# Performance work log

Measured on AMD Instinct MI355X. Metric: run time of the kernel, lower is better.

The kernel has to match this reference:

```python
import jax, jax.numpy as jnp
import numpy as np

EPS = 1e-5

def _ln(x, g, b):
    mu = jnp.mean(x, axis=-1, keepdims=True)
    var = jnp.mean((x - mu) ** 2, axis=-1, keepdims=True)
    return (x - mu) * jax.lax.rsqrt(var + EPS) * g + b

B, SQ, SK, C, H = 4, 1024, 2048, 1024, 16
DH = C // H          # head_dim (latent_dim == in_dim)
L = C                # latent_dim

def setup_inputs() -> dict:
    key = jax.random.key(0)
    ks = list(jax.random.split(key, 16))
    s = 0.02
    d = {
        'queries': jax.random.normal(ks[0], (B, SQ, C), jnp.float32),
        'contexts': jax.random.normal(ks[1], (B, SK, C), jnp.float32),
        # SelfAttention params
        'sa_ln_g': jnp.ones((C,), jnp.float32),
        'sa_ln_b': jnp.zeros((C,), jnp.float32),
        'sa_qkv_w': jax.random.normal(ks[2], (2 * L + C, C), jnp.float32) * s,  # torch Linear weight (out,in)
        'sa_out_w': jax.random.normal(ks[3], (C, C), jnp.float32) * s,
        'sa_out_b': jnp.zeros((C,), jnp.float32),
        # Cross Attention params
        'ca_ln_g': jnp.ones((C,), jnp.float32),
        'ca_ln_b': jnp.zeros((C,), jnp.float32),
        'ca_q_w': jax.random.normal(ks[4], (L, C), jnp.float32) * s,
        'ca_k_w': jax.random.normal(ks[5], (L, C), jnp.float32) * s,
        'ca_v_w': jax.random.normal(ks[6], (C, C), jnp.float32) * s,
        'ca_out_w': jax.random.normal(ks[7], (C, C), jnp.float32) * s,
        'ca_out_b': jnp.zeros((C,), jnp.float32),
        # FFN (linear block) params
        'ff_ln1_g': jnp.ones((C,), jnp.float32),
        'ff_ln1_b': jnp.zeros((C,), jnp.float32),
        'ff_w1': jax.random.normal(ks[8], (2 * C, C), jnp.float32) * s,
        'ff_ln2_g': jnp.ones((2 * C,), jnp.float32),
        'ff_ln2_b': jnp.zeros((2 * C,), jnp.float32),
        'ff_w2': jax.random.normal(ks[9], (C, 2 * C), jnp.float32) * s,
    }
    return d

def _forward(queries, contexts, sa_ln_g, sa_ln_b, sa_qkv_w, sa_out_w, sa_out_b,
             ca_ln_g, ca_ln_b, ca_q_w, ca_k_w, ca_v_w, ca_out_w, ca_out_b,
             ff_ln1_g, ff_ln1_b, ff_w1, ff_ln2_g, ff_ln2_b, ff_w2):
    scale = 1.0 / jnp.sqrt(jnp.float32(C))  # note: module scales by sqrt(C), not sqrt(head_dim)
    # ---- SelfAttention ----
    x = queries
    h = _ln(x, sa_ln_g, sa_ln_b)
    qkv = (h @ sa_qkv_w.T).reshape(B, SQ, H, -1)  # (B,SQ,H, 2*DH + C//H)
    q, k, v = jnp.split(qkv, [DH, 2 * DH], axis=-1)
    e = jnp.einsum('nqhc,nkhc->nhqk', q, k)
    a = jax.nn.softmax(e * scale, axis=-1)
    o = jnp.einsum('nhql,nlhc->nqhc', a, v).reshape(B, SQ, C)
    x = o @ sa_out_w.T + sa_out_b + x
    # ---- Cross Attention ----
    qpre = x
    hq = _ln(x, ca_ln_g, ca_ln_b)
    q = (hq @ ca_q_w.T).reshape(B, SQ, H, DH)
    k = (contexts @ ca_k_w.T).reshape(B, SK, H, DH)
    v = (contexts @ ca_v_w.T).reshape(B, SK, H, C // H)
    energy = jnp.einsum('nqhc,nkhc->nhqk', q, k)  # (B,H,SQ,SK)
    a = jax.nn.softmax(energy * scale, axis=-1)
    o = jnp.einsum('nhql,nlhc->nqhc', a, v).reshape(B, SQ, C)
    x = o @ ca_out_w.T + ca_out_b + qpre
    # ---- FFN: LN -> SiLU -> Linear -> LN -> SiLU -> Linear, residual ----
    f = jax.nn.silu(_ln(x, ff_ln1_g, ff_ln1_b))
    f = f @ ff_w1.T
    f = jax.nn.silu(_ln(f, ff_ln2_g, ff_ln2_b))
    f = f @ ff_w2.T
    out = x + f  # dropout p=0 -> identity
    return out, energy

def reference(queries, contexts, sa_ln_g, sa_ln_b, sa_qkv_w, sa_out_w, sa_out_b,
              ca_ln_g, ca_ln_b, ca_q_w, ca_k_w, ca_v_w, ca_out_w, ca_out_b,
              ff_ln1_g, ff_ln1_b, ff_w1, ff_ln2_g, ff_ln2_b, ff_w2):
    return _forward(queries, contexts, sa_ln_g, sa_ln_b, sa_qkv_w, sa_out_w, sa_out_b,
                    ca_ln_g, ca_ln_b, ca_q_w, ca_k_w, ca_v_w, ca_out_w, ca_out_b,
                    ff_ln1_g, ff_ln1_b, ff_w1, ff_ln2_g, ff_ln2_b, ff_w2)
```

## Files before the change

### kernel.cpp

```cpp
#include <hip/hip_runtime.h>
#include <hip/hip_bf16.h>
#include <math.h>


namespace {
constexpr int BB  = 4;
constexpr int SQ_ = 1024;
constexpr int SK_ = 2048;
constexpr int CC  = 1024;
constexpr int HH  = 16;
constexpr float SCALE  = 0.03125f;
constexpr float LN_EPS = 1e-5f;
}

typedef __hip_bfloat16 bf16;
typedef __attribute__((ext_vector_type(8))) short short8;
typedef __attribute__((ext_vector_type(4))) float f32x4;

__device__ __forceinline__ void gload16(const void* g, void* l) {
    __builtin_amdgcn_global_load_lds((const __attribute__((address_space(1))) unsigned int*)g,
                                     (__attribute__((address_space(3))) unsigned int*)l,
                                     16, 0, 0);
}

#define MAXJOBS 10
struct CvtJobs {
    const float* src[MAXJOBS];
    bf16*        dst[MAXJOBS];
    int          end[MAXJOBS];
    int          njobs;
};

__global__ __launch_bounds__(256)
void cvt_all(CvtJobs J) {
    const int i = blockIdx.x * 256 + threadIdx.x;
    if (i >= J.end[J.njobs - 1]) return;
    int j = 0;
    while (i >= J.end[j]) ++j;
    const int base = j ? J.end[j - 1] : 0;
    const int k = i - base;
    const float4 a = ((const float4*)J.src[j])[2 * k];
    const float4 b = ((const float4*)J.src[j])[2 * k + 1];
    union { ushort4 v; bf16 h[4]; } lo, hi;
    lo.h[0] = __float2bfloat16(a.x); lo.h[1] = __float2bfloat16(a.y);
    lo.h[2] = __float2bfloat16(a.z); lo.h[3] = __float2bfloat16(a.w);
    hi.h[0] = __float2bfloat16(b.x); hi.h[1] = __float2bfloat16(b.y);
    hi.h[2] = __float2bfloat16(b.z); hi.h[3] = __float2bfloat16(b.w);
    ((ushort4*)J.dst[j])[2 * k]     = lo.v;
    ((ushort4*)J.dst[j])[2 * k + 1] = hi.v;
}

__device__ __forceinline__ float4 ld4(const float* p, int idx) {
    return ((const float4*)p)[idx];
}
__device__ __forceinline__ float4 ld4(const bf16* p, int idx) {
    const ushort4 u = ((const ushort4*)p)[idx];
    float4 r;
    r.x = __bfloat162float(*(const bf16*)&u.x);
    r.y = __bfloat162float(*(const bf16*)&u.y);
    r.z = __bfloat162float(*(const bf16*)&u.z);
    r.w = __bfloat162float(*(const bf16*)&u.w);
    return r;
}

template<int NCOLS, typename TI>
__global__ __launch_bounds__(256)
void ln_kernel(const TI* __restrict__ x, const float* __restrict__ g,
               const float* __restrict__ b, bf16* __restrict__ out, int do_silu) {
    constexpr int PER = NCOLS / 1024;
    const size_t row = blockIdx.x;
    const TI* xr = x + row * NCOLS;
    float4 vals[PER];
    float s = 0.f, ss = 0.f;
#pragma unroll
    for (int i = 0; i < PER; ++i) {
        vals[i] = ld4(xr, threadIdx.x + i * 256);
        s  += vals[i].x + vals[i].y + vals[i].z + vals[i].w;
        ss += vals[i].x * vals[i].x + vals[i].y * vals[i].y
            + vals[i].z * vals[i].z + vals[i].w * vals[i].w;
    }
    for (int off = 32; off > 0; off >>= 1) {
        s  += __shfl_down(s, off, 64);
        ss += __shfl_down(ss, off, 64);
    }
    __shared__ float red[10];
    const int wid = threadIdx.x >> 6, lane = threadIdx.x & 63;
    if (lane == 0) { red[wid] = s; red[wid + 4] = ss; }
    __syncthreads();
    if (threadIdx.x == 0) {
        const float ts  = red[0] + red[1] + red[2] + red[3];
        const float tss = red[4] + red[5] + red[6] + red[7];
        const float mu  = ts / NCOLS;
        const float var = tss / NCOLS - mu * mu;
        red[8] = mu;
        red[9] = rsqrtf(var + LN_EPS);
    }
    __syncthreads();
    const float mu = red[8], rstd = red[9];
    bf16* outr = out + row * NCOLS;
#pragma unroll
    for (int i = 0; i < PER; ++i) {
        const int c = (threadIdx.x + i * 256) * 4;
        const float4 gg = *(const float4*)(g + c);
        const float4 bb = *(const float4*)(b + c);
        float y0 = (vals[i].x - mu) * rstd * gg.x + bb.x;
        float y1 = (vals[i].y - mu) * rstd * gg.y + bb.y;
        float y2 = (vals[i].z - mu) * rstd * gg.z + bb.z;
        float y3 = (vals[i].w - mu) * rstd * gg.w + bb.w;
        if (do_silu) {
            y0 = y0 / (1.f + __expf(-y0));
            y1 = y1 / (1.f + __expf(-y1));
            y2 = y2 / (1.f + __expf(-y2));
            y3 = y3 / (1.f + __expf(-y3));
        }
        union { ushort4 v; bf16 h[4]; } pk;
        pk.h[0] = __float2bfloat16(y0); pk.h[1] = __float2bfloat16(y1);
        pk.h[2] = __float2bfloat16(y2); pk.h[3] = __float2bfloat16(y3);
        *(ushort4*)(outr + c) = pk.v;
    }
}

template<int OUT16, int BMT, int VMODE>
__global__ __launch_bounds__(256)
void gemm_bt16(const bf16* __restrict__ A, const bf16* __restrict__ B,
               void* __restrict__ Cv, int M, int N, int K,
               const float* __restrict__ bias, const float* __restrict__ resid,
               bf16* __restrict__ Vt, int ldt) {
    constexpr int WC = (BMT == 128) ? 2 : 4;
    constexpr int NF = (BMT == 128) ? 4 : 2;
    __shared__ bf16 As[2][BMT * 32];
    __shared__ bf16 Bs[2][128 * 32];
    const int tid  = threadIdx.x;
    const int lane = tid & 63;
    const int w    = tid >> 6;
    const int wr = w / WC, wc = w % WC;

    const int nwg = gridDim.x * gridDim.y;
    const int bid = blockIdx.x + gridDim.x * blockIdx.y;
    const int logical = (bid & 7) * (nwg >> 3) + (bid >> 3);
    const int m0 = (logical / gridDim.x) * BMT;
    const int n0 = (logical % gridDim.x) * 128;

    f32x4 acc[4][NF] = {};

    const int srow = tid >> 2;
    const int scol = (tid & 3) * 8;
    const bf16* Ap  = A + (size_t)(m0 + srow) * K + scol;
    const bf16* Ap2 = Ap + (size_t)64 * K;
    const bf16* Bp  = B + (size_t)(n0 + srow) * K + scol;
    const bf16* Bp2 = Bp + (size_t)64 * K;

    const int arow = wr * 64 + (lane & 15);
    const int brow = wc * (NF * 16) + (lane & 15);
    const int kgrp = (lane >> 4) * 16;

    auto stage = [&](int buf, int k0) {
        char* AsB = (char*)As[buf] + w * 1024;
        char* BsB = (char*)Bs[buf] + w * 1024;
        gload16(Ap  + k0, AsB);
        if (BMT == 128) gload16(Ap2 + k0, AsB + 4096);
        gload16(Bp  + k0, BsB);
        gload16(Bp2 + k0, BsB + 4096);
    };

    const int nt = K >> 5;
    stage(0, 0);
    __syncthreads();
    for (int t = 0; t < nt; ++t) {
        if (t + 1 < nt) stage((t + 1) & 1, (t + 1) << 5);
        const char* Ab = (const char*)As[t & 1];
        const char* Bb = (const char*)Bs[t & 1];
        short8 aF[4], bF[NF];
#pragma unroll
        for (int m = 0; m < 4; ++m)
            aF[m] = *(const short8*)(Ab + ((arow + m * 16) * 64 + kgrp));
#pragma unroll
        for (int n = 0; n < NF; ++n)
            bF[n] = *(const short8*)(Bb + ((brow + n * 16) * 64 + kgrp));
#pragma unroll
        for (int m = 0; m < 4; ++m)
#pragma unroll
            for (int n = 0; n < NF; ++n)
                acc[m][n] = __builtin_amdgcn_mfma_f32_16x16x32_bf16(aF[m], bF[n], acc[m][n], 0, 0, 0);
        __syncthreads();
    }

    const int crow0 = m0 + wr * 64 + (lane >> 4) * 4;
    const int ccol0 = n0 + wc * (NF * 16) + (lane & 15);
#pragma unroll
    for (int m = 0; m < 4; ++m) {
#pragma unroll
        for (int n = 0; n < NF; ++n) {
            const int col = ccol0 + n * 16;
            const int row0 = crow0 + m * 16;
            if (OUT16) {
                int vrow = -1;
                if (VMODE == 1) {
                    const int r = col % 192;
                    if (r >= 128) vrow = (col / 192) * 64 + r - 128;
                } else if (VMODE == 2) {
                    if (col >= 1024) vrow = col - 1024;
                }
                union { ushort4 v; bf16 h[4]; } pk;
#pragma unroll
                for (int j = 0; j < 4; ++j) pk.h[j] = __float2bfloat16(acc[m][n][j]);
                if (VMODE && vrow >= 0) {
                    *(ushort4*)(Vt + (size_t)vrow * ldt + row0) = pk.v;
                } else {
#pragma unroll
                    for (int j = 0; j < 4; ++j)
                        ((bf16*)Cv)[(size_t)(row0 + j) * N + col] = pk.h[j];
                }
            } else {
                const float bv = bias ? bias[col] : 0.f;
#pragma unroll
                for (int j = 0; j < 4; ++j) {
                    const int row = row0 + j;
                    float v = acc[m][n][j] + bv;
                    if (resid) v += resid[(size_t)row * N + col];
                    ((float*)Cv)[(size_t)row * N + col] = v;
                }
            }
        }
    }
}

template<bool ENERGY>
__global__ __launch_bounds__(256, 4)
void flash_attn(const bf16* __restrict__ Qb, int ldq, int qh_str,
                const bf16* __restrict__ Kb, int ldk, int kh_str, int kh_add,
                const bf16* __restrict__ Vt, int ldvt,
                bf16* __restrict__ O, float* __restrict__ energy,
                int SKV, int SQl, float scale) {
    __shared__ bf16 P[64][136];
    const int tid = threadIdx.x;
    const int lane = tid & 63, wid = tid >> 6;
    const int l15 = lane & 15, l4 = lane >> 4;

    const int gx  = gridDim.x;
    const int nwg = gx * gridDim.y;
    const int bid = blockIdx.x + gx * blockIdx.y;
    const int logical = (bid & 7) * (nwg >> 3) + (bid >> 3);
    const int xq = logical % gx;
    const int z  = logical / gx;

    const int b = z >> 4, h = z & 15;
    const int q0 = xq * 64;

    const bf16* Qp = Qb + (size_t)b * SQl * ldq + (size_t)h * qh_str;
    const bf16* Kp = Kb + (size_t)b * SKV * ldk + (size_t)h * kh_str + kh_add;
    const bf16* Vp = Vt + (size_t)h * 64 * ldvt + (size_t)b * SKV;

    short8 aQ[2];
#pragma unroll
    for (int s = 0; s < 2; ++s)
        aQ[s] = *(const short8*)(Qp + (size_t)(q0 + wid * 16 + l15) * ldq + s * 32 + l4 * 8);

    f32x4 oacc[4] = {};
    float mI = -1e30f, lI = 0.f;

    for (int kv0 = 0; kv0 < SKV; kv0 += 64) {
        f32x4 sa[4] = {};
        __builtin_amdgcn_s_setprio(1);
#pragma unroll
        for (int n = 0; n < 4; ++n) {
            const bf16* kr = Kp + (size_t)(kv0 + n * 16 + l15) * ldk + l4 * 8;
            const short8 b0 = *(const short8*)(kr);
            const short8 b1 = *(const short8*)(kr + 32);
            sa[n] = __builtin_amdgcn_mfma_f32_16x16x32_bf16(b0, aQ[0], sa[n], 0, 0, 0);
            sa[n] = __builtin_amdgcn_mfma_f32_16x16x32_bf16(b1, aQ[1], sa[n], 0, 0, 0);
        }
        __builtin_amdgcn_s_setprio(0);
        if (ENERGY) {
            float* er = energy + (size_t)z * SQl * SKV
                      + (size_t)(q0 + wid * 16 + l15) * SKV + kv0 + l4 * 4;
#pragma unroll
            for (int n = 0; n < 4; ++n)
                __builtin_nontemporal_store(sa[n], (f32x4*)(er + n * 16));
        }
        float mx = fmaxf(fmaxf(fmaxf(sa[0][0], sa[0][1]), fmaxf(sa[0][2], sa[0][3])),
                         fmaxf(fmaxf(sa[1][0], sa[1][1]), fmaxf(sa[1][2], sa[1][3])));
        mx = fmaxf(mx, fmaxf(fmaxf(sa[2][0], sa[2][1]), fmaxf(sa[2][2], sa[2][3])));
        mx = fmaxf(mx, fmaxf(fmaxf(sa[3][0], sa[3][1]), fmaxf(sa[3][2], sa[3][3])));
        mx *= scale;
        mx = fmaxf(mx, __shfl_xor(mx, 16, 64));
        mx = fmaxf(mx, __shfl_xor(mx, 32, 64));
        if (__any(mx > mI)) {
            const float nm = fmaxf(mI, mx);
            const float f = __expf(mI - nm);
            mI = nm;
            lI *= f;
#pragma unroll
            for (int j = 0; j < 4; ++j) {
                const float fj = __shfl(f, l4 * 4 + j, 64);
#pragma unroll
                for (int n = 0; n < 4; ++n) oacc[n][j] *= fj;
            }
        }
        float rs = 0.f;
#pragma unroll
        for (int n = 0; n < 4; ++n)
#pragma unroll
            for (int j = 0; j < 4; ++j) {
                const float p = __expf(sa[n][j] * scale - mI);
                sa[n][j] = p;
                rs += p;
            }
        rs += __shfl_xor(rs, 16, 64);
        rs += __shfl_xor(rs, 32, 64);
        lI += rs;
#pragma unroll
        for (int n = 0; n < 4; ++n) {
            union { ushort4 v; bf16 hh[4]; } pk;
            pk.hh[0] = __float2bfloat16(sa[n][0]);
            pk.hh[1] = __float2bfloat16(sa[n][1]);
            pk.hh[2] = __float2bfloat16(sa[n][2]);
            pk.hh[3] = __float2bfloat16(sa[n][3]);
            *(ushort4*)(&P[wid * 16 + l15][n * 16 + l4 * 4]) = pk.v;
        }
        __builtin_amdgcn_s_setprio(1);
#pragma unroll
        for (int ks = 0; ks < 2; ++ks) {
            const short8 aP = *(const short8*)(&P[wid * 16 + l15][ks * 32 + l4 * 8]);
#pragma unroll
            for (int n = 0; n < 4; ++n) {
                const short8 bV = *(const short8*)(Vp + (size_t)(n * 16 + l15) * ldvt + kv0 + ks * 32 + l4 * 8);
                oacc[n] = __builtin_amdgcn_mfma_f32_16x16x32_bf16(aP, bV, oacc[n], 0, 0, 0);
            }
        }
        __builtin_amdgcn_s_setprio(0);
    }
#pragma unroll
    for (int j = 0; j < 4; ++j) {
        const float lj = __shfl(lI, l4 * 4 + j, 64);
        const float rl = 1.f / lj;
        const size_t row = (size_t)b * SQl + q0 + wid * 16 + l4 * 4 + j;
#pragma unroll
        for (int n = 0; n < 4; ++n)
            O[row * 1024 + h * 64 + n * 16 + l15] = __float2bfloat16(oacc[n][j] * rl);
    }
}

extern "C" void kernel_launch(void* const* d_in, const int* in_sizes, int n_in,
                              void* d_out, int out_size, void* d_ws, size_t ws_size,
                              hipStream_t stream) {
    const float* queries  = (const float*)d_in[0];
    const float* contexts = (const float*)d_in[1];
    const float* sa_ln_g  = (const float*)d_in[2];
    const float* sa_ln_b  = (const float*)d_in[3];
    const float* sa_qkv_w = (const float*)d_in[4];
    const float* sa_out_w = (const float*)d_in[5];
    const float* sa_out_b = (const float*)d_in[6];
    const float* ca_ln_g  = (const float*)d_in[7];
    const float* ca_ln_b  = (const float*)d_in[8];
    const float* ca_q_w   = (const float*)d_in[9];
    const float* ca_k_w   = (const float*)d_in[10];
    const float* ca_v_w   = (const float*)d_in[11];
    const float* ca_out_w = (const float*)d_in[12];
    const float* ca_out_b = (const float*)d_in[13];
    const float* ff_ln1_g = (const float*)d_in[14];
    const float* ff_ln1_b = (const float*)d_in[15];
    const float* ff_w1    = (const float*)d_in[16];
    const float* ff_ln2_g = (const float*)d_in[17];
    const float* ff_ln2_b = (const float*)d_in[18];
    const float* ff_w2    = (const float*)d_in[19];

    float* out    = (float*)d_out;
    float* energy = out + (size_t)BB * SQ_ * CC;

    const size_t MEG = 1024 * 1024;

    float* ws = (float*)d_ws;
    bf16*  X0_16      = (bf16*)ws;
    bf16*  o16        = (bf16*)(ws + 4 * MEG);
    bf16*  ca_out_w16 = (bf16*)(ws + 6 * MEG);
    bf16*  ff_w1_16   = (bf16*)(ws + (13 * MEG) / 2);
    bf16*  ff_w2_16   = (bf16*)(ws + (15 * MEG) / 2);
    bf16*  q_ca16     = (bf16*)(ws + (17 * MEG) / 2);
    bf16*  KV_ca      = (bf16*)(ws + (21 * MEG) / 2);
    bf16*  Vt_ca      = (bf16*)(ws + (37 * MEG) / 2);
    float* E_buf      = ws + (45 * MEG) / 2;
    float* C_buf      = ws + (53 * MEG) / 2;
    bf16*  C_buf16    = (bf16*)C_buf;

    bf16* EZ         = (bf16*)energy;
    bf16* ctx16      = EZ;
    bf16* qkv16      = EZ + 8  * MEG;
    bf16* Vt_sa      = EZ + 20 * MEG;
    bf16* qkv_w16    = EZ + 24 * MEG;
    bf16* sa_out_w16 = EZ + 27 * MEG;
    bf16* ca_q_w16   = EZ + 28 * MEG;
    bf16* ca_k_w16   = EZ + 29 * MEG;
    bf16* ca_v_w16   = EZ + 30 * MEG;

    const int M1 = BB * SQ_;
    const int M2 = BB * SK_;
    const dim3 thr(256);

    {
        CvtJobs J;
        const float* srcs[9] = { sa_qkv_w, sa_out_w, ca_q_w, ca_k_w, ca_v_w,
                                 ca_out_w, ff_w1, ff_w2, contexts };
        bf16* dsts[9] = { qkv_w16, sa_out_w16, ca_q_w16, ca_k_w16, ca_v_w16,
                          ca_out_w16, ff_w1_16, ff_w2_16, ctx16 };
        const size_t ns[9] = { 3 * MEG, 1 * MEG, 1 * MEG, 1 * MEG, 1 * MEG,
                               1 * MEG, 2 * MEG, 2 * MEG, 8 * MEG };
        int acc_n8 = 0;
        for (int j = 0; j < 9; ++j) {
            J.src[j] = srcs[j];
            J.dst[j] = dsts[j];
            acc_n8 += (int)(ns[j] / 8);
            J.end[j] = acc_n8;
        }
        J.njobs = 9;
        cvt_all<<<(acc_n8 + 255) / 256, thr, 0, stream>>>(J);
    }

    ln_kernel<1024, float><<<M1, thr, 0, stream>>>(queries, sa_ln_g, sa_ln_b, X0_16, 0);
    gemm_bt16<1, 128, 1><<<dim3(3072 / 128, M1 / 128), thr, 0, stream>>>(
        X0_16, qkv_w16, qkv16, M1, 3072, 1024, nullptr, nullptr, Vt_sa, M1);
    flash_attn<false><<<dim3(SQ_ / 64, BB * HH), thr, 0, stream>>>(
        qkv16, 3072, 192, qkv16, 3072, 192, 64, Vt_sa, M1,
        o16, nullptr, SQ_, SQ_, SCALE);
    gemm_bt16<0, 64, 0><<<dim3(1024 / 128, M1 / 64), thr, 0, stream>>>(
        o16, sa_out_w16, E_buf, M1, CC, CC, sa_out_b, queries, nullptr, 0);

    ln_kernel<1024, float><<<M1, thr, 0, stream>>>(E_buf, ca_ln_g, ca_ln_b, X0_16, 0);
    gemm_bt16<1, 64, 0><<<dim3(1024 / 128, M1 / 64), thr, 0, stream>>>(
        X0_16, ca_q_w16, q_ca16, M1, CC, CC, nullptr, nullptr, nullptr, 0);
    gemm_bt16<1, 128, 2><<<dim3(2048 / 128, M2 / 128), thr, 0, stream>>>(
        ctx16, ca_k_w16, KV_ca, M2, 2048, 1024, nullptr, nullptr, Vt_ca, M2);
    flash_attn<true><<<dim3(SQ_ / 64, BB * HH), thr, 0, stream>>>(
        q_ca16, 1024, 64, KV_ca, 2048, 64, 0, Vt_ca, M2,
        o16, energy, SK_, SQ_, SCALE);
    gemm_bt16<0, 64, 0><<<dim3(1024 / 128, M1 / 64), thr, 0, stream>>>(
        o16, ca_out_w16, E_buf, M1, CC, CC, ca_out_b, E_buf, nullptr, 0);

    ln_kernel<1024, float><<<M1, thr, 0, stream>>>(E_buf, ff_ln1_g, ff_ln1_b, X0_16, 1);
    gemm_bt16<1, 64, 0><<<dim3(2048 / 128, M1 / 64), thr, 0, stream>>>(
        X0_16, ff_w1_16, C_buf16, M1, 2048, 1024, nullptr, nullptr, nullptr, 0);
    ln_kernel<2048, bf16><<<M1, thr, 0, stream>>>(C_buf16, ff_ln2_g, ff_ln2_b, X0_16, 1);
    gemm_bt16<0, 64, 0><<<dim3(1024 / 128, M1 / 64), thr, 0, stream>>>(
        X0_16, ff_w2_16, out, M1, CC, 2048, nullptr, E_buf, nullptr, 0);
}
```

Baseline: 646.5 us.

## Merge QKV and cross-attention KV GEMMs into one launch; store residual stream in bf16

Adds a gemm_dual kernel that runs the self-attention QKV projection and the cross-attention K/V projection in a single grid, so the two independent GEMMs share one launch and fill the GPU together. The fp32 intermediate residual buffer is replaced with a bf16 buffer (E16): the output GEMMs write bf16 and read the residual as bf16, and the LayerNorms read bf16. This cuts launch count and memory traffic on the residual path. The cost is lower precision in the residual stream, which accumulates rounding across the block.

```diff
diff --git a/kernel.cpp b/kernel.cpp
--- a/kernel.cpp
+++ b/kernel.cpp
@@ -120,12 +120,12 @@
     }
 }
 
-template<int OUT16, int BMT, int VMODE>
+template<int OUTF, int BMT>
 __global__ __launch_bounds__(256)
 void gemm_bt16(const bf16* __restrict__ A, const bf16* __restrict__ B,
                void* __restrict__ Cv, int M, int N, int K,
-               const float* __restrict__ bias, const float* __restrict__ resid,
-               bf16* __restrict__ Vt, int ldt) {
+               const float* __restrict__ bias, const float* __restrict__ residF,
+               const bf16* __restrict__ residH) {
     constexpr int WC = (BMT == 128) ? 2 : 4;
     constexpr int NF = (BMT == 128) ? 4 : 2;
     __shared__ bf16 As[2][BMT * 32];
@@ -193,33 +193,112 @@
         for (int n = 0; n < NF; ++n) {
             const int col = ccol0 + n * 16;
             const int row0 = crow0 + m * 16;
-            if (OUT16) {
-                int vrow = -1;
-                if (VMODE == 1) {
-                    const int r = col % 192;
-                    if (r >= 128) vrow = (col / 192) * 64 + r - 128;
-                } else if (VMODE == 2) {
-                    if (col >= 1024) vrow = col - 1024;
-                }
-                union { ushort4 v; bf16 h[4]; } pk;
-#pragma unroll
-                for (int j = 0; j < 4; ++j) pk.h[j] = __float2bfloat16(acc[m][n][j]);
-                if (VMODE && vrow >= 0) {
-                    *(ushort4*)(Vt + (size_t)vrow * ldt + row0) = pk.v;
-                } else {
-#pragma unroll
-                    for (int j = 0; j < 4; ++j)
-                        ((bf16*)Cv)[(size_t)(row0 + j) * N + col] = pk.h[j];
-                }
+            const float bv = bias ? bias[col] : 0.f;
+#pragma unroll
+            for (int j = 0; j < 4; ++j) {
+                const int row = row0 + j;
+                float v = acc[m][n][j] + bv;
+                if (residF) v += residF[(size_t)row * N + col];
+                if (residH) v += __bfloat162float(residH[(size_t)row * N + col]);
+                if (OUTF) ((bf16*)Cv)[(size_t)row * N + col] = __float2bfloat16(v);
+                else      ((float*)Cv)[(size_t)row * N + col] = v;
+            }
+        }
+    }
+}
+
+struct GJob {
+    const bf16* A; const bf16* B; bf16* C; bf16* Vt;
+    int N, nx, ldt, vmode;
+};
+
+__global__ __launch_bounds__(256)
+void gemm_dual(GJob j0, GJob j1, int blocks0) {
+    constexpr int K = 1024;
+    __shared__ bf16 As[2][128 * 32];
+    __shared__ bf16 Bs[2][128 * 32];
+    const int tid  = threadIdx.x;
+    const int lane = tid & 63;
+    const int w    = tid >> 6;
+    const int wr = w >> 1, wc = w & 1;
+
+    const int nwg = gridDim.x;
+    const int bid = blockIdx.x;
+    const int logical = (bid & 7) * (nwg >> 3) + (bid >> 3);
+    const bool first = logical < blocks0;
+    const GJob j = first ? j0 : j1;
+    const int lid = first ? logical : logical - blocks0;
+    const int m0 = (lid / j.nx) * 128;
+    const int n0 = (lid % j.nx) * 128;
+
+    f32x4 acc[4][4] = {};
+
+    const int srow = tid >> 2;
+    const int scol = (tid & 3) * 8;
+    const bf16* Ap  = j.A + (size_t)(m0 + srow) * K + scol;
+    const bf16* Ap2 = Ap + (size_t)64 * K;
+    const bf16* Bp  = j.B + (size_t)(n0 + srow) * K + scol;
+    const bf16* Bp2 = Bp + (size_t)64 * K;
+
+    const int arow = wr * 64 + (lane & 15);
+    const int brow = wc * 64 + (lane & 15);
+    const int kgrp = (lane >> 4) * 16;
+
+    auto stage = [&](int buf, int k0) {
+        char* AsB = (char*)As[buf] + w * 1024;
+        char* BsB = (char*)Bs[buf] + w * 1024;
+        gload16(Ap  + k0, AsB);
+        gload16(Ap2 + k0, AsB + 4096);
+        gload16(Bp  + k0, BsB);
+        gload16(Bp2 + k0, BsB + 4096);
+    };
+
+    const int nt = K >> 5;
+    stage(0, 0);
+    __syncthreads();
+    for (int t = 0; t < nt; ++t) {
+        if (t + 1 < nt) stage((t + 1) & 1, (t + 1) << 5);
+        const char* Ab = (const char*)As[t & 1];
+        const char* Bb = (const char*)Bs[t & 1];
+        short8 aF[4], bF[4];
+#pragma unroll
+        for (int m = 0; m < 4; ++m)
+            aF[m] = *(const short8*)(Ab + ((arow + m * 16) * 64 + kgrp));
+#pragma unroll
+        for (int n = 0; n < 4; ++n)
+            bF[n] = *(const short8*)(Bb + ((brow + n * 16) * 64 + kgrp));
+#pragma unroll
+        for (int m = 0; m < 4; ++m)
+#pragma unroll
+            for (int n = 0; n < 4; ++n)
+                acc[m][n] = __builtin_amdgcn_mfma_f32_16x16x32_bf16(aF[m], bF[n], acc[m][n], 0, 0, 0);
+        __syncthreads();
+    }
+
+    const int crow0 = m0 + wr * 64 + (lane >> 4) * 4;
+    const int ccol0 = n0 + wc * 64 + (lane & 15);
+#pragma unroll
+    for (int m = 0; m < 4; ++m) {
+#pragma unroll
+        for (int n = 0; n < 4; ++n) {
+            const int col = ccol0 + n * 16;
+            const int row0 = crow0 + m * 16;
+            int vrow = -1;
+            if (j.vmode == 1) {
+                const int r = col % 192;
+                if (r >= 128) vrow = (col / 192) * 64 + r - 128;
             } else {
-                const float bv = bias ? bias[col] : 0.f;
-#pragma unroll
-                for (int j = 0; j < 4; ++j) {
-                    const int row = row0 + j;
-                    float v = acc[m][n][j] + bv;
-                    if (resid) v += resid[(size_t)row * N + col];
-                    ((float*)Cv)[(size_t)row * N + col] = v;
-                }
+                if (col >= 1024) vrow = col - 1024;
+            }
+            union { ushort4 v; bf16 h[4]; } pk;
+#pragma unroll
+            for (int jj = 0; jj < 4; ++jj) pk.h[jj] = __float2bfloat16(acc[m][n][jj]);
+            if (vrow >= 0) {
+                *(ushort4*)(j.Vt + (size_t)vrow * j.ldt + row0) = pk.v;
+            } else {
+#pragma unroll
+                for (int jj = 0; jj < 4; ++jj)
+                    j.C[(size_t)(row0 + jj) * j.N + col] = pk.h[jj];
             }
         }
     }
@@ -379,9 +458,8 @@
     bf16*  q_ca16     = (bf16*)(ws + (17 * MEG) / 2);
     bf16*  KV_ca      = (bf16*)(ws + (21 * MEG) / 2);
     bf16*  Vt_ca      = (bf16*)(ws + (37 * MEG) / 2);
-    float* E_buf      = ws + (45 * MEG) / 2;
-    float* C_buf      = ws + (53 * MEG) / 2;
-    bf16*  C_buf16    = (bf16*)C_buf;
+    bf16*  E16        = (bf16*)(ws + (45 * MEG) / 2);
+    bf16*  C_buf16    = (bf16*)(ws + (53 * MEG) / 2);
 
     bf16* EZ         = (bf16*)energy;
     bf16* ctx16      = EZ;
@@ -417,29 +495,32 @@
     }
 
     ln_kernel<1024, float><<<M1, thr, 0, stream>>>(queries, sa_ln_g, sa_ln_b, X0_16, 0);
-    gemm_bt16<1, 128, 1><<<dim3(3072 / 128, M1 / 128), thr, 0, stream>>>(
-        X0_16, qkv_w16, qkv16, M1, 3072, 1024, nullptr, nullptr, Vt_sa, M1);
+    {
+        GJob jq = { X0_16, qkv_w16, qkv16, Vt_sa, 3072, 24, M1, 1 };
+        GJob jk = { ctx16, ca_k_w16, KV_ca, Vt_ca, 2048, 16, M2, 2 };
+        const int blocks0 = 24 * (M1 / 128);
+        const int blocks1 = 16 * (M2 / 128);
+        gemm_dual<<<blocks0 + blocks1, thr, 0, stream>>>(jq, jk, blocks0);
+    }
     flash_attn<false><<<dim3(SQ_ / 64, BB * HH), thr, 0, stream>>>(
         qkv16, 3072, 192, qkv16, 3072, 192, 64, Vt_sa, M1,
         o16, nullptr, SQ_, SQ_, SCALE);
-    gemm_bt16<0, 64, 0><<<dim3(1024 / 128, M1 / 64), thr, 0, stream>>>(
-        o16, sa_out_w16, E_buf, M1, CC, CC, sa_out_b, queries, nullptr, 0);
-
-    ln_kernel<1024, float><<<M1, thr, 0, stream>>>(E_buf, ca_ln_g, ca_ln_b, X0_16, 0);
-    gemm_bt16<1, 64, 0><<<dim3(1024 / 128, M1 / 64), thr, 0, stream>>>(
-        X0_16, ca_q_w16, q_ca16, M1, CC, CC, nullptr, nullptr, nullptr, 0);
-    gemm_bt16<1, 128, 2><<<dim3(2048 / 128, M2 / 128), thr, 0, stream>>>(
-        ctx16, ca_k_w16, KV_ca, M2, 2048, 1024, nullptr, nullptr, Vt_ca, M2);
+    gemm_bt16<1, 64><<<dim3(1024 / 128, M1 / 64), thr, 0, stream>>>(
+        o16, sa_out_w16, E16, M1, CC, CC, sa_out_b, queries, nullptr);
+
+    ln_kernel<1024, bf16><<<M1, thr, 0, stream>>>(E16, ca_ln_g, ca_ln_b, X0_16, 0);
+    gemm_bt16<1, 64><<<dim3(1024 / 128, M1 / 64), thr, 0, stream>>>(
+        X0_16, ca_q_w16, q_ca16, M1, CC, CC, nullptr, nullptr, nullptr);
     flash_attn<true><<<dim3(SQ_ / 64, BB * HH), thr, 0, stream>>>(
         q_ca16, 1024, 64, KV_ca, 2048, 64, 0, Vt_ca, M2,
         o16, energy, SK_, SQ_, SCALE);
-    gemm_bt16<0, 64, 0><<<dim3(1024 / 128, M1 / 64), thr, 0, stream>>>(
-        o16, ca_out_w16, E_buf, M1, CC, CC, ca_out_b, E_buf, nullptr, 0);
-
-    ln_kernel<1024, float><<<M1, thr, 0, stream>>>(E_buf, ff_ln1_g, ff_ln1_b, X0_16, 1);
-    gemm_bt16<1, 64, 0><<<dim3(2048 / 128, M1 / 64), thr, 0, stream>>>(
-        X0_16, ff_w1_16, C_buf16, M1, 2048, 1024, nullptr, nullptr, nullptr, 0);
+    gemm_bt16<1, 64><<<dim3(1024 / 128, M1 / 64), thr, 0, stream>>>(
+        o16, ca_out_w16, E16, M1, CC, CC, ca_out_b, nullptr, E16);
+
+    ln_kernel<1024, bf16><<<M1, thr, 0, stream>>>(E16, ff_ln1_g, ff_ln1_b, X0_16, 1);
+    gemm_bt16<1, 64><<<dim3(2048 / 128, M1 / 64), thr, 0, stream>>>(
+        X0_16, ff_w1_16, C_buf16, M1, 2048, 1024, nullptr, nullptr, nullptr);
     ln_kernel<2048, bf16><<<M1, thr, 0, stream>>>(C_buf16, ff_ln2_g, ff_ln2_b, X0_16, 1);
-    gemm_bt16<0, 64, 0><<<dim3(1024 / 128, M1 / 64), thr, 0, stream>>>(
-        X0_16, ff_w2_16, out, M1, CC, 2048, nullptr, E_buf, nullptr, 0);
-}
+    gemm_bt16<0, 64><<<dim3(1024 / 128, M1 / 64), thr, 0, stream>>>(
+        X0_16, ff_w2_16, out, M1, CC, 2048, nullptr, nullptr, E16);
+}
```

Result: no change. 653.1 us (+1.0%).

## Store residual stream in bf16, use exp2 softmax, reorder context KV projection

Applied to the files above, without the earlier changes.

The residual activations between blocks (E_buf) are now kept in bf16 instead of fp32. This halves traffic for the residual reads and writes, and the LayerNorm kernels read bf16. The softmax folds log2(e) into the scale and uses exp2f in place of __expf. The context K/V projection GEMM is launched earlier, before self-attention. The bf16 residual adds rounding error at each residual step and may hurt accuracy against the fp32 reference.

```diff
diff --git a/kernel.cpp b/kernel.cpp
--- a/kernel.cpp
+++ b/kernel.cpp
@@ -9,7 +9,7 @@
 constexpr int SK_ = 2048;
 constexpr int CC  = 1024;
 constexpr int HH  = 16;
-constexpr float SCALE  = 0.03125f;
+constexpr float SCALE2 = 0.03125f * 1.44269504089f;
 constexpr float LN_EPS = 1e-5f;
 }
 
@@ -120,12 +120,12 @@
     }
 }
 
-template<int OUT16, int BMT, int VMODE>
+template<int OUTF, int BMT, int VMODE>
 __global__ __launch_bounds__(256)
 void gemm_bt16(const bf16* __restrict__ A, const bf16* __restrict__ B,
                void* __restrict__ Cv, int M, int N, int K,
-               const float* __restrict__ bias, const float* __restrict__ resid,
-               bf16* __restrict__ Vt, int ldt) {
+               const float* __restrict__ bias, const float* __restrict__ residF,
+               const bf16* __restrict__ residH, bf16* __restrict__ Vt, int ldt) {
     constexpr int WC = (BMT == 128) ? 2 : 4;
     constexpr int NF = (BMT == 128) ? 4 : 2;
     __shared__ bf16 As[2][BMT * 32];
@@ -193,7 +193,7 @@
         for (int n = 0; n < NF; ++n) {
             const int col = ccol0 + n * 16;
             const int row0 = crow0 + m * 16;
-            if (OUT16) {
+            if (OUTF) {
                 int vrow = -1;
                 if (VMODE == 1) {
                     const int r = col % 192;
@@ -201,15 +201,21 @@
                 } else if (VMODE == 2) {
                     if (col >= 1024) vrow = col - 1024;
                 }
-                union { ushort4 v; bf16 h[4]; } pk;
-#pragma unroll
-                for (int j = 0; j < 4; ++j) pk.h[j] = __float2bfloat16(acc[m][n][j]);
                 if (VMODE && vrow >= 0) {
+                    union { ushort4 v; bf16 h[4]; } pk;
+#pragma unroll
+                    for (int j = 0; j < 4; ++j) pk.h[j] = __float2bfloat16(acc[m][n][j]);
                     *(ushort4*)(Vt + (size_t)vrow * ldt + row0) = pk.v;
                 } else {
-#pragma unroll
-                    for (int j = 0; j < 4; ++j)
-                        ((bf16*)Cv)[(size_t)(row0 + j) * N + col] = pk.h[j];
+                    const float bv = bias ? bias[col] : 0.f;
+#pragma unroll
+                    for (int j = 0; j < 4; ++j) {
+                        const int row = row0 + j;
+                        float v = acc[m][n][j] + bv;
+                        if (residF) v += residF[(size_t)row * N + col];
+                        if (residH) v += __bfloat162float(residH[(size_t)row * N + col]);
+                        ((bf16*)Cv)[(size_t)row * N + col] = __float2bfloat16(v);
+                    }
                 }
             } else {
                 const float bv = bias ? bias[col] : 0.f;
@@ -217,7 +223,8 @@
                 for (int j = 0; j < 4; ++j) {
                     const int row = row0 + j;
                     float v = acc[m][n][j] + bv;
-                    if (resid) v += resid[(size_t)row * N + col];
+                    if (residF) v += residF[(size_t)row * N + col];
+                    if (residH) v += __bfloat162float(residH[(size_t)row * N + col]);
                     ((float*)Cv)[(size_t)row * N + col] = v;
                 }
             }
@@ -231,7 +238,7 @@
                 const bf16* __restrict__ Kb, int ldk, int kh_str, int kh_add,
                 const bf16* __restrict__ Vt, int ldvt,
                 bf16* __restrict__ O, float* __restrict__ energy,
-                int SKV, int SQl, float scale) {
+                int SKV, int SQl, float scale2) {
     __shared__ bf16 P[64][136];
     const int tid = threadIdx.x;
     const int lane = tid & 63, wid = tid >> 6;
@@ -282,12 +289,12 @@
                          fmaxf(fmaxf(sa[1][0], sa[1][1]), fmaxf(sa[1][2], sa[1][3])));
         mx = fmaxf(mx, fmaxf(fmaxf(sa[2][0], sa[2][1]), fmaxf(sa[2][2], sa[2][3])));
         mx = fmaxf(mx, fmaxf(fmaxf(sa[3][0], sa[3][1]), fmaxf(sa[3][2], sa[3][3])));
-        mx *= scale;
+        mx *= scale2;
         mx = fmaxf(mx, __shfl_xor(mx, 16, 64));
         mx = fmaxf(mx, __shfl_xor(mx, 32, 64));
         if (__any(mx > mI)) {
             const float nm = fmaxf(mI, mx);
-            const float f = __expf(mI - nm);
+            const float f = exp2f(mI - nm);
             mI = nm;
             lI *= f;
 #pragma unroll
@@ -302,7 +309,7 @@
         for (int n = 0; n < 4; ++n)
 #pragma unroll
             for (int j = 0; j < 4; ++j) {
-                const float p = __expf(sa[n][j] * scale - mI);
+                const float p = exp2f(sa[n][j] * scale2 - mI);
                 sa[n][j] = p;
                 rs += p;
             }
@@ -379,9 +386,8 @@
     bf16*  q_ca16     = (bf16*)(ws + (17 * MEG) / 2);
     bf16*  KV_ca      = (bf16*)(ws + (21 * MEG) / 2);
     bf16*  Vt_ca      = (bf16*)(ws + (37 * MEG) / 2);
-    float* E_buf      = ws + (45 * MEG) / 2;
-    float* C_buf      = ws + (53 * MEG) / 2;
-    bf16*  C_buf16    = (bf16*)C_buf;
+    bf16*  E16        = (bf16*)(ws + (45 * MEG) / 2);
+    bf16*  C_buf16    = (bf16*)(ws + (53 * MEG) / 2);
 
     bf16* EZ         = (bf16*)energy;
     bf16* ctx16      = EZ;
@@ -418,28 +424,28 @@
 
     ln_kernel<1024, float><<<M1, thr, 0, stream>>>(queries, sa_ln_g, sa_ln_b, X0_16, 0);
     gemm_bt16<1, 128, 1><<<dim3(3072 / 128, M1 / 128), thr, 0, stream>>>(
-        X0_16, qkv_w16, qkv16, M1, 3072, 1024, nullptr, nullptr, Vt_sa, M1);
+        X0_16, qkv_w16, qkv16, M1, 3072, 1024, nullptr, nullptr, nullptr, Vt_sa, M1);
+    gemm_bt16<1, 128, 2><<<dim3(2048 / 128, M2 / 128), thr, 0, stream>>>(
+        ctx16, ca_k_w16, KV_ca, M2, 2048, 1024, nullptr, nullptr, nullptr, Vt_ca, M2);
     flash_attn<false><<<dim3(SQ_ / 64, BB * HH), thr, 0, stream>>>(
         qkv16, 3072, 192, qkv16, 3072, 192, 64, Vt_sa, M1,
-        o16, nullptr, SQ_, SQ_, SCALE);
-    gemm_bt16<0, 64, 0><<<dim3(1024 / 128, M1 / 64), thr, 0, stream>>>(
-        o16, sa_out_w16, E_buf, M1, CC, CC, sa_out_b, queries, nullptr, 0);
-
-    ln_kernel<1024, float><<<M1, thr, 0, stream>>>(E_buf, ca_ln_g, ca_ln_b, X0_16, 0);
+        o16, nullptr, SQ_, SQ_, SCALE2);
     gemm_bt16<1, 64, 0><<<dim3(1024 / 128, M1 / 64), thr, 0, stream>>>(
-        X0_16, ca_q_w16, q_ca16, M1, CC, CC, nullptr, nullptr, nullptr, 0);
-    gemm_bt16<1, 128, 2><<<dim3(2048 / 128, M2 / 128), thr, 0, stream>>>(
-        ctx16, ca_k_w16, KV_ca, M2, 2048, 1024, nullptr, nullptr, Vt_ca, M2);
+        o16, sa_out_w16, E16, M1, CC, CC, sa_out_b, queries, nullptr, nullptr, 0);
+
+    ln_kernel<1024, bf16><<<M1, thr, 0, stream>>>(E16, ca_ln_g, ca_ln_b, X0_16, 0);
+    gemm_bt16<1, 64, 0><<<dim3(1024 / 128, M1 / 64), thr, 0, stream>>>(
+        X0_16, ca_q_w16, q_ca16, M1, CC, CC, nullptr, nullptr, nullptr, nullptr, 0);
     flash_attn<true><<<dim3(SQ_ / 64, BB * HH), thr, 0, stream>>>(
         q_ca16, 1024, 64, KV_ca, 2048, 64, 0, Vt_ca, M2,
-        o16, energy, SK_, SQ_, SCALE);
-    gemm_bt16<0, 64, 0><<<dim3(1024 / 128, M1 / 64), thr, 0, stream>>>(
-        o16, ca_out_w16, E_buf, M1, CC, CC, ca_out_b, E_buf, nullptr, 0);
-
-    ln_kernel<1024, float><<<M1, thr, 0, stream>>>(E_buf, ff_ln1_g, ff_ln1_b, X0_16, 1);
+        o16, energy, SK_, SQ_, SCALE2);
+    gemm_bt16<1, 64, 0><<<dim3(1024 / 128, M1 / 64), thr, 0, stream>>>(
+        o16, ca_out_w16, E16, M1, CC, CC, ca_out_b, nullptr, E16, nullptr, 0);
+
+    ln_kernel<1024, bf16><<<M1, thr, 0, stream>>>(E16, ff_ln1_g, ff_ln1_b, X0_16, 1);
     gemm_bt16<1, 64, 0><<<dim3(2048 / 128, M1 / 64), thr, 0, stream>>>(
-        X0_16, ff_w1_16, C_buf16, M1, 2048, 1024, nullptr, nullptr, nullptr, 0);
+        X0_16, ff_w1_16, C_buf16, M1, 2048, 1024, nullptr, nullptr, nullptr, nullptr, 0);
     ln_kernel<2048, bf16><<<M1, thr, 0, stream>>>(C_buf16, ff_ln2_g, ff_ln2_b, X0_16, 1);
     gemm_bt16<0, 64, 0><<<dim3(1024 / 128, M1 / 64), thr, 0, stream>>>(
-        X0_16, ff_w2_16, out, M1, CC, 2048, nullptr, E_buf, nullptr, 0);
-}
+        X0_16, ff_w2_16, out, M1, CC, 2048, nullptr, nullptr, E16, nullptr, 0);
+}
```

New measurement: 661.5 us. +2.3%, slower.
